# Optimization experiments

Measured on AMD Instinct MI355X. Metric: run time of the kernel, lower is better.

## Reference

```python
import jax, jax.numpy as jnp
import numpy as np

N_NODES = 100000
N_EDGES = 1600000
IN_C, HID_C, OUT_C = 128, 128, 64


def setup_inputs() -> dict:
    key = jax.random.key(0)
    ks = jax.random.split(key, 9)
    features = jax.random.normal(ks[0], (N_NODES, IN_C), dtype=jnp.float32)
    src = jax.random.randint(ks[1], (N_EDGES,), 0, N_NODES, dtype=jnp.int32)
    dst = jax.random.randint(ks[2], (N_EDGES,), 0, N_NODES, dtype=jnp.int32)
    def glorot(k, fan_in, fan_out):
        lim = float(np.sqrt(6.0 / (fan_in + fan_out)))
        return jax.random.uniform(k, (fan_in, fan_out), jnp.float32, -lim, lim)
    return {
        "features": features, "src": src, "dst": dst,
        "W1": glorot(ks[3], IN_C, HID_C), "b1": jnp.zeros((HID_C,), jnp.float32),
        "W2": glorot(ks[4], HID_C, HID_C), "b2": jnp.zeros((HID_C,), jnp.float32),
        "W3": glorot(ks[5], HID_C, OUT_C), "b3": jnp.zeros((OUT_C,), jnp.float32),
    }


def _graph_conv(x, src, dst, W, b, inv_sqrt_out, inv_sqrt_in):
    # DGL GraphConv, norm='both': h = D_in^{-1/2} A D_out^{-1/2} (x W) + b
    h = (x * inv_sqrt_out[:, None]) @ W            # [N, out]
    agg = jax.ops.segment_sum(h[src], dst, num_segments=N_NODES)
    return agg * inv_sqrt_in[:, None] + b


def reference(features, src, dst, W1, b1, W2, b2, W3, b3):
    ones = jnp.ones((N_EDGES,), jnp.float32)
    deg_out = jnp.clip(jax.ops.segment_sum(ones, src, num_segments=N_NODES), 1.0)
    deg_in = jnp.clip(jax.ops.segment_sum(ones, dst, num_segments=N_NODES), 1.0)
    iso, isi = deg_out ** -0.5, deg_in ** -0.5
    x = jax.nn.relu(_graph_conv(features, src, dst, W1, b1, iso, isi))
    x = jax.nn.relu(_graph_conv(x, src, dst, W2, b2, iso, isi))
    x = _graph_conv(x, src, dst, W3, b3, iso, isi)
    return jax.nn.log_softmax(x, axis=1)
```

## Files before the change

kernel.cpp:

```cpp
#include <hip/hip_runtime.h>
#include <hip/hip_bf16.h>

#define IN_C 128
#define HID_C 128
#define OUT_C 64

typedef unsigned short u16;
typedef unsigned int   u32;
typedef __attribute__((ext_vector_type(8))) short short8;
typedef __attribute__((ext_vector_type(4))) float f32x4;
typedef __attribute__((ext_vector_type(2))) float f32x2;

__device__ __forceinline__ u16 bf16_bits(float x) {
    __hip_bfloat16 h = __float2bfloat16(x);
    return *(u16*)&h;
}
__device__ __forceinline__ void split_hi_lo(float a, u16& hi, u16& lo) {
    __hip_bfloat16 h = __float2bfloat16(a);
    float hf = __bfloat162float(h);
    __hip_bfloat16 l = __float2bfloat16(a - hf);
    hi = *(u16*)&h; lo = *(u16*)&l;
}
__device__ __forceinline__ void pk_acc(f32x2& acc, u32 v) {
    f32x2 val;
    val.x = __uint_as_float(v << 16);
    val.y = __uint_as_float(v & 0xffff0000u);
    asm("v_pk_add_f32 %0, %0, %1" : "+v"(acc) : "v"(val));
}


__global__ __launch_bounds__(256)
void part_hist(const int* __restrict__ keys, int* __restrict__ bh,
               int E, int K, int NB) {
    const int b = blockIdx.x;
    extern __shared__ int lh[];
    for (int i = threadIdx.x; i < K; i += 256) lh[i] = 0;
    __syncthreads();
    const int lo = (int)((long long)E * b / NB);
    const int hi = (int)((long long)E * (b + 1) / NB);
    for (int i = lo + threadIdx.x; i < hi; i += 256)
        atomicAdd(&lh[keys[i] >> 8], 1);
    __syncthreads();
    for (int k = threadIdx.x; k < K; k += 256)
        bh[k * NB + b] = lh[k];
}

template <bool PACK>
__global__ __launch_bounds__(256)
void part_scatter(const int* __restrict__ keys, const int* __restrict__ other,
                  const int* __restrict__ ofs, u32* __restrict__ out,
                  int E, int K, int NB) {
    const int b = blockIdx.x;
    extern __shared__ int lcur[];
    for (int k = threadIdx.x; k < K; k += 256) lcur[k] = ofs[k * NB + b];
    __syncthreads();
    const int lo = (int)((long long)E * b / NB);
    const int hi = (int)((long long)E * (b + 1) / NB);
    for (int i = lo + threadIdx.x; i < hi; i += 256) {
        int key = keys[i];
        int p = atomicAdd(&lcur[key >> 8], 1);
        out[p] = PACK ? (((u32)other[i] << 8) | (u32)(key & 255)) : (u32)key;
    }
}

__global__ __launch_bounds__(256)
void bucket_count(const u32* __restrict__ pairs, const int* __restrict__ ofs,
                  int* __restrict__ cnt, int N, int NB, int K, int cap) {
    const int k = blockIdx.x;
    __shared__ int lc[256];
    lc[threadIdx.x] = 0;
    __syncthreads();
    const int s0 = ofs[k * NB];
    const int s1 = (k == K - 1) ? cap : ofs[(k + 1) * NB];
    for (int i = s0 + threadIdx.x; i < s1; i += 256)
        atomicAdd(&lc[pairs[i] & 255], 1);
    __syncthreads();
    const int node = k * 256 + threadIdx.x;
    if (node < N) cnt[node] = lc[threadIdx.x];
}

__global__ __launch_bounds__(256)
void bucket_fill(const u32* __restrict__ pairs, const int* __restrict__ ofs,
                 const int* __restrict__ row_start, int* __restrict__ csr,
                 int N, int NB, int K, int E) {
    const int k = blockIdx.x;
    __shared__ int lcur[256];
    const int node = k * 256 + threadIdx.x;
    lcur[threadIdx.x] = (node < N) ? row_start[node] : 0;
    __syncthreads();
    const int s0 = ofs[k * NB];
    const int s1 = (k == K - 1) ? E : ofs[(k + 1) * NB];
    for (int i = s0 + threadIdx.x; i < s1; i += 256) {
        u32 pr = pairs[i];
        int p = atomicAdd(&lcur[pr & 255], 1);
        csr[p] = (int)(pr >> 8);
    }
}


__global__ __launch_bounds__(256)
void scan_pass1(const int* __restrict__ in, int* __restrict__ blocksum, int M) {
    const int b = blockIdx.x, t = threadIdx.x;
    const int base = b * 1024 + t * 4;
    int s = 0;
#pragma unroll
    for (int j = 0; j < 4; ++j) {
        int idx = base + j;
        if (idx < M) s += in[idx];
    }
#pragma unroll
    for (int off = 32; off >= 1; off >>= 1) s += __shfl_xor(s, off);
    __shared__ int wsum[4];
    if ((t & 63) == 0) wsum[t >> 6] = s;
    __syncthreads();
    if (t == 0) blocksum[b] = wsum[0] + wsum[1] + wsum[2] + wsum[3];
}

__global__ __launch_bounds__(1024)
void scan_g2(int* __restrict__ a, int nb) {
    __shared__ int s[1024];
    const int t = threadIdx.x;
    int v = (t < nb) ? a[t] : 0;
    s[t] = v;
    __syncthreads();
    for (int off = 1; off < 1024; off <<= 1) {
        int x = (t >= off) ? s[t - off] : 0;
        __syncthreads();
        s[t] += x;
        __syncthreads();
    }
    if (t < nb) a[t] = s[t] - v;
}

__global__ __launch_bounds__(256)
void scan_g3(const int* __restrict__ in, const int* __restrict__ blockoff,
             int* __restrict__ out, int M) {
    __shared__ int ssum[256];
    const int b = blockIdx.x, t = threadIdx.x;
    const int base = b * 1024 + t * 4;
    int c[4];
#pragma unroll
    for (int j = 0; j < 4; ++j) {
        int idx = base + j;
        c[j] = (idx < M) ? in[idx] : 0;
    }
    const int tot = c[0] + c[1] + c[2] + c[3];
    ssum[t] = tot;
    __syncthreads();
    for (int off = 1; off < 256; off <<= 1) {
        int v = (t >= off) ? ssum[t - off] : 0;
        __syncthreads();
        ssum[t] += v;
        __syncthreads();
    }
    int run = blockoff[b] + ssum[t] - tot;
#pragma unroll
    for (int j = 0; j < 4; ++j) {
        int idx = base + j;
        if (idx < M) { out[idx] = run; run += c[j]; }
    }
}

__global__ __launch_bounds__(256)
void scan_pass3n(const int* __restrict__ cnt_in, const int* __restrict__ cnt_out,
                 const int* __restrict__ blockoff, int* __restrict__ row_start,
                 float* __restrict__ iso, float* __restrict__ isi, int N, int E) {
    __shared__ int ssum[256];
    const int b = blockIdx.x, t = threadIdx.x;
    const int base = b * 1024 + t * 4;
    int c[4];
#pragma unroll
    for (int j = 0; j < 4; ++j) {
        int idx = base + j;
        c[j] = (idx < N) ? cnt_in[idx] : 0;
    }
    const int tot = c[0] + c[1] + c[2] + c[3];
    ssum[t] = tot;
    __syncthreads();
    for (int off = 1; off < 256; off <<= 1) {
        int v = (t >= off) ? ssum[t - off] : 0;
        __syncthreads();
        ssum[t] += v;
        __syncthreads();
    }
    int run = blockoff[b] + ssum[t] - tot;
#pragma unroll
    for (int j = 0; j < 4; ++j) {
        int idx = base + j;
        if (idx < N) {
            row_start[idx] = run;
            run += c[j];
            int di = c[j] < 1 ? 1 : c[j];
            int co = cnt_out[idx];
            int dd = co < 1 ? 1 : co;
            isi[idx] = rsqrtf((float)di);
            iso[idx] = rsqrtf((float)dd);
        }
    }
    if (b == 0 && t == 0) row_start[N] = E;
}


__global__ __launch_bounds__(128)
void wt_prep_all(const float* __restrict__ W1, const float* __restrict__ W2,
                 const float* __restrict__ W3, u16* __restrict__ Wt1,
                 u16* __restrict__ Wt2, u16* __restrict__ Wt3) {
    const int b = blockIdx.x, k = threadIdx.x;
    if (b < 128)       Wt1[b * 128 + k] = bf16_bits(W1[k * 128 + b]);
    else if (b < 256)  { int c = b - 128; Wt2[c * 128 + k] = bf16_bits(W2[k * 128 + c]); }
    else               { int c = b - 256; Wt3[c * 128 + k] = bf16_bits(W3[k * 64 + c]); }
}

template <int C>
__device__ __forceinline__
void mfma_store(const u16* sAh, const u16* sAl, const u16* __restrict__ Wt,
                u16* __restrict__ H, int row0, int N, int t) {
    constexpr int NT = C / 16;
    const int wid = t >> 6, lane = t & 63;
    const int r0 = wid * 16;
    const int arow = r0 + (lane & 15);
    const int kb = (lane >> 4) * 8;

    f32x4 acc[NT];
#pragma unroll
    for (int i = 0; i < NT; ++i) acc[i] = (f32x4){0.f, 0.f, 0.f, 0.f};

    const u16* wbase = Wt + (size_t)(lane & 15) * 128 + kb;

#pragma unroll
    for (int kk = 0; kk < 4; ++kk) {
        short8 ah = *(const short8*)(&sAh[arow * 136 + kk * 32 + kb]);
        short8 al = *(const short8*)(&sAl[arow * 136 + kk * 32 + kb]);
#pragma unroll
        for (int ct = 0; ct < NT; ++ct) {
            short8 bf = *(const short8*)(wbase + ct * 16 * 128 + kk * 32);
            acc[ct] = __builtin_amdgcn_mfma_f32_16x16x32_bf16(ah, bf, acc[ct], 0, 0, 0);
            acc[ct] = __builtin_amdgcn_mfma_f32_16x16x32_bf16(al, bf, acc[ct], 0, 0, 0);
        }
    }

    const int rbase = row0 + r0 + (lane >> 4) * 4;
#pragma unroll
    for (int ct = 0; ct < NT; ++ct) {
        int gcol = ct * 16 + (lane & 15);
#pragma unroll
        for (int r = 0; r < 4; ++r) {
            int grow = rbase + r;
            if (grow < N) H[(size_t)grow * C + gcol] = bf16_bits(acc[ct][r]);
        }
    }
}


__global__ __launch_bounds__(256)
void gemm1_fused(const float* __restrict__ X, const float* __restrict__ iso,
                 const u16* __restrict__ Wt, u16* __restrict__ H, int N) {
    __shared__ u16 sAh[64 * 136];
    __shared__ u16 sAl[64 * 136];
    const int t = threadIdx.x;
    const int row0 = blockIdx.x * 64;

    for (int i = t; i < 2048; i += 256) {
        int r = i >> 5, kv = (i & 31) << 2;
        int gr = row0 + r;
        if (gr >= N) gr = N - 1;
        float s = iso[gr];
        float4 x = *(const float4*)(X + (size_t)gr * 128 + kv);
        u16 h0, l0, h1, l1, h2, l2, h3, l3;
        split_hi_lo(x.x * s, h0, l0);
        split_hi_lo(x.y * s, h1, l1);
        split_hi_lo(x.z * s, h2, l2);
        split_hi_lo(x.w * s, h3, l3);
        uint2 hp = make_uint2((u32)h0 | ((u32)h1 << 16), (u32)h2 | ((u32)h3 << 16));
        uint2 lp = make_uint2((u32)l0 | ((u32)l1 << 16), (u32)l2 | ((u32)l3 << 16));
        *(uint2*)(&sAh[r * 136 + kv]) = hp;
        *(uint2*)(&sAl[r * 136 + kv]) = lp;
    }
    __syncthreads();
    mfma_store<128>(sAh, sAl, Wt, H, row0, N, t);
}


template <int C>
__global__ __launch_bounds__(256)
void gemm_mfma(const u16* __restrict__ Ah, const u16* __restrict__ Al,
               const u16* __restrict__ Wt, u16* __restrict__ H, int N) {
    __shared__ u16 sAh[64 * 136];
    __shared__ u16 sAl[64 * 136];
    const int t = threadIdx.x;
    const int row0 = blockIdx.x * 64;

    for (int c = t; c < 1024; c += 256) {
        int r = c >> 4, kc = c & 15;
        int gr = row0 + r;
        if (gr >= N) gr = N - 1;
        *(uint4*)(&sAh[r * 136 + kc * 8]) = *(const uint4*)(Ah + (size_t)gr * 128 + kc * 8);
        *(uint4*)(&sAl[r * 136 + kc * 8]) = *(const uint4*)(Al + (size_t)gr * 128 + kc * 8);
    }
    __syncthreads();
    mfma_store<C>(sAh, sAl, Wt, H, row0, N, t);
}


__device__ __forceinline__
f32x2 gather128(const u16* __restrict__ Hin, const int* __restrict__ csr_src,
                int rs, int re, int lane) {
    f32x2 acc; acc.x = 0.f; acc.y = 0.f;
    int e = rs;
    while (e < re) {
        int nloc = re - e;
        if (nloc > 64) nloc = 64;
        int idx = (lane < nloc) ? csr_src[e + lane] : 0;
        int j = 0;
        for (; j + 16 <= nloc; j += 16) {
            u32 v[16];
#pragma unroll
            for (int q = 0; q < 16; ++q) {
                int s = __builtin_amdgcn_readlane(idx, j + q);
                v[q] = *(const u32*)(Hin + (size_t)s * 128 + lane * 2);
            }
#pragma unroll
            for (int q = 0; q < 16; ++q) pk_acc(acc, v[q]);
        }
        for (; j + 4 <= nloc; j += 4) {
            u32 v[4];
#pragma unroll
            for (int q = 0; q < 4; ++q) {
                int s = __builtin_amdgcn_readlane(idx, j + q);
                v[q] = *(const u32*)(Hin + (size_t)s * 128 + lane * 2);
            }
#pragma unroll
            for (int q = 0; q < 4; ++q) pk_acc(acc, v[q]);
        }
        for (; j < nloc; ++j) {
            int s = __builtin_amdgcn_readlane(idx, j);
            pk_acc(acc, *(const u32*)(Hin + (size_t)s * 128 + lane * 2));
        }
        e += nloc;
    }
    return acc;
}


__global__ __launch_bounds__(256)
void agg_relu(const u16* __restrict__ H, const int* __restrict__ row_start,
              const int* __restrict__ csr_src, const float* __restrict__ isi,
              const float* __restrict__ iso, const float* __restrict__ bias,
              u16* __restrict__ Ah, u16* __restrict__ Al, int N) {
    const int wid  = (int)((blockIdx.x * (size_t)blockDim.x + threadIdx.x) >> 6);
    const int lane = threadIdx.x & 63;
    if (wid >= N) return;
    const int rs = row_start[wid];
    const int re = row_start[wid + 1];

    f32x2 acc = gather128(H, csr_src, rs, re, lane);

    float2 b = *(const float2*)(bias + lane * 2);
    const float sc = isi[wid], so = iso[wid];
    float o0 = fmaxf(acc.x * sc + b.x, 0.f) * so;
    float o1 = fmaxf(acc.y * sc + b.y, 0.f) * so;
    u16 h0, l0, h1, l1;
    split_hi_lo(o0, h0, l0);
    split_hi_lo(o1, h1, l1);
    ((u32*)Ah)[(size_t)wid * 64 + lane] = (u32)h0 | ((u32)h1 << 16);
    ((u32*)Al)[(size_t)wid * 64 + lane] = (u32)l0 | ((u32)l1 << 16);
}


__global__ __launch_bounds__(256)
void agg_final(const u16* __restrict__ H, const int* __restrict__ row_start,
               const int* __restrict__ csr_src, const float* __restrict__ isi,
               const float* __restrict__ bias, float* __restrict__ Out, int N) {
    const int wid  = (int)((blockIdx.x * (size_t)blockDim.x + threadIdx.x) >> 6);
    const int lane = threadIdx.x & 63;
    if (wid >= N) return;
    const int rs = row_start[wid];
    const int re = row_start[wid + 1];
    const float sc = isi[wid];

    float a = 0.f;
    int e = rs;
    while (e < re) {
        int nloc = re - e;
        if (nloc > 64) nloc = 64;
        int idx = (lane < nloc) ? csr_src[e + lane] : 0;
        int j = 0;
        for (; j + 8 <= nloc; j += 8) {
            u32 v[8];
#pragma unroll
            for (int q = 0; q < 8; ++q) {
                int s = __builtin_amdgcn_readlane(idx, j + q);
                v[q] = H[(size_t)s * 64 + lane];
            }
#pragma unroll
            for (int q = 0; q < 8; ++q) a += __uint_as_float(v[q] << 16);
        }
        for (; j + 4 <= nloc; j += 4) {
            u32 v[4];
#pragma unroll
            for (int q = 0; q < 4; ++q) {
                int s = __builtin_amdgcn_readlane(idx, j + q);
                v[q] = H[(size_t)s * 64 + lane];
            }
#pragma unroll
            for (int q = 0; q < 4; ++q) a += __uint_as_float(v[q] << 16);
        }
        for (; j < nloc; ++j) {
            int s = __builtin_amdgcn_readlane(idx, j);
            a += __uint_as_float((u32)H[(size_t)s * 64 + lane] << 16);
        }
        e += nloc;
    }
    float v = a * sc + bias[lane];
    float m = v;
#pragma unroll
    for (int off = 32; off >= 1; off >>= 1) m = fmaxf(m, __shfl_xor(m, off));
    float ex = expf(v - m);
    float ss = ex;
#pragma unroll
    for (int off = 32; off >= 1; off >>= 1) ss += __shfl_xor(ss, off);
    v = (v - m) - logf(ss);
    Out[(size_t)wid * 64 + lane] = v;
}


extern "C" void kernel_launch(void* const* d_in, const int* in_sizes, int n_in,
                              void* d_out, int out_size, void* d_ws, size_t ws_size,
                              hipStream_t stream) {
    const float* features = (const float*)d_in[0];
    const int*   src      = (const int*)d_in[1];
    const int*   dst      = (const int*)d_in[2];
    const float* W1       = (const float*)d_in[3];
    const float* b1       = (const float*)d_in[4];
    const float* W2       = (const float*)d_in[5];
    const float* b2       = (const float*)d_in[6];
    const float* W3       = (const float*)d_in[7];
    const float* b3       = (const float*)d_in[8];
    float*       out      = (float*)d_out;

    const int N  = in_sizes[0] / IN_C;
    const int E  = in_sizes[1];
    const int K  = (N + 255) >> 8;
    const int NB = 256;
    const int M  = 2 * K * NB;
    const int nbe = (M + 1023) / 1024;
    const int nb  = (N + 1023) / 1024;

    char* ws = (char*)d_ws;
    const size_t SLOT = 400128;
    int*   cnt_out   = (int*)(ws + 0 * SLOT);
    int*   cnt_in    = (int*)(ws + 1 * SLOT);
    int*   row_start = (int*)(ws + 2 * SLOT);
    float* iso       = (float*)(ws + 3 * SLOT);
    float* isi       = (float*)(ws + 4 * SLOT);
    int*   blocksum  = (int*)(ws + 5 * SLOT);
    int*   eblocksum = blocksum + 2048;
    int*   csr       = (int*)(ws + 6 * SLOT);
    char*  p         = ws + 6 * SLOT + 6400000;
    int*   BH        = (int*)p;
    int*   OFS       = (int*)(p + 1000000);
    u32*   pairs     = (u32*)(p + 2000000);
    u16*   Hb        = (u16*)(p + 14800000);
    u16*   Ah        = (u16*)(p + 40400000);
    u16*   Al        = (u16*)(p + 66000000);
    u16*   Wt1       = (u16*)(p + 91600000);
    u16*   Wt2       = Wt1 + 128 * 128;
    u16*   Wt3       = Wt2 + 128 * 128;

    const size_t ldsK = (size_t)K * sizeof(int);

    part_hist<<<NB, 256, ldsK, stream>>>(dst, BH,           E, K, NB);
    part_hist<<<NB, 256, ldsK, stream>>>(src, BH + K * NB,  E, K, NB);
    scan_pass1<<<nbe, 256, 0, stream>>>(BH, eblocksum, M);
    scan_g2<<<1, 1024, 0, stream>>>(eblocksum, nbe);
    scan_g3<<<nbe, 256, 0, stream>>>(BH, eblocksum, OFS, M);
    part_scatter<true ><<<NB, 256, ldsK, stream>>>(dst, src, OFS,          pairs, E, K, NB);
    part_scatter<false><<<NB, 256, ldsK, stream>>>(src, src, OFS + K * NB, pairs, E, K, NB);
    bucket_count<<<K, 256, 0, stream>>>(pairs, OFS,          cnt_in,  N, NB, K, E);
    bucket_count<<<K, 256, 0, stream>>>(pairs, OFS + K * NB, cnt_out, N, NB, K, 2 * E);
    scan_pass1<<<nb, 256, 0, stream>>>(cnt_in, blocksum, N);
    scan_g2<<<1, 1024, 0, stream>>>(blocksum, nb);
    scan_pass3n<<<nb, 256, 0, stream>>>(cnt_in, cnt_out, blocksum, row_start, iso, isi, N, E);
    bucket_fill<<<K, 256, 0, stream>>>(pairs, OFS, row_start, csr, N, NB, K, E);

    wt_prep_all<<<320, 128, 0, stream>>>(W1, W2, W3, Wt1, Wt2, Wt3);

    const int gblocks = (N + 63) / 64;
    const int ablocks = (int)(((size_t)N * 64 + 255) / 256);

    gemm1_fused<<<gblocks, 256, 0, stream>>>(features, iso, Wt1, Hb, N);
    agg_relu<<<ablocks, 256, 0, stream>>>(Hb, row_start, csr, isi, iso, b1, Ah, Al, N);
    gemm_mfma<128><<<gblocks, 256, 0, stream>>>(Ah, Al, Wt2, Hb, N);
    agg_relu<<<ablocks, 256, 0, stream>>>(Hb, row_start, csr, isi, iso, b2, Ah, Al, N);
    gemm_mfma<64><<<gblocks, 256, 0, stream>>>(Ah, Al, Wt3, Hb, N);
    agg_final<<<ablocks, 256, 0, stream>>>(Hb, row_start, csr, isi, b3, out, N);
}
```

Baseline: 373.0 us.

## Merge src/dst partition kernels and reuse bucket offsets for row starts

Fuses the src and dst histogram, scatter and bucket-count kernels into single launches that process both key arrays per pass. The separate scan of in-degree counts is dropped: row starts are taken from the bucket offsets already computed (OFS at bucket b*4), so two scan launches disappear. The change also adds nontemporal loads and stores on streaming data and unrolls the final aggregation gather to 16. Together these cut launch count and redundant passes over the edge arrays, at the cost of more LDS per block in the fused partition kernels.

Measured after the change: 378.2 us. Within noise of the previous version (+1.4%).

```diff
diff --git a/kernel.cpp b/kernel.cpp
--- a/kernel.cpp
+++ b/kernel.cpp
@@ -30,43 +30,57 @@
 
 
 __global__ __launch_bounds__(256)
-void part_hist(const int* __restrict__ keys, int* __restrict__ bh,
-               int E, int K, int NB) {
+void part_hist2(const int* __restrict__ src, const int* __restrict__ dst,
+                int* __restrict__ bh, int E, int K, int NB) {
     const int b = blockIdx.x;
     extern __shared__ int lh[];
-    for (int i = threadIdx.x; i < K; i += 256) lh[i] = 0;
-    __syncthreads();
-    const int lo = (int)((long long)E * b / NB);
-    const int hi = (int)((long long)E * (b + 1) / NB);
-    for (int i = lo + threadIdx.x; i < hi; i += 256)
-        atomicAdd(&lh[keys[i] >> 8], 1);
-    __syncthreads();
-    for (int k = threadIdx.x; k < K; k += 256)
-        bh[k * NB + b] = lh[k];
-}
-
-template <bool PACK>
-__global__ __launch_bounds__(256)
-void part_scatter(const int* __restrict__ keys, const int* __restrict__ other,
-                  const int* __restrict__ ofs, u32* __restrict__ out,
-                  int E, int K, int NB) {
-    const int b = blockIdx.x;
-    extern __shared__ int lcur[];
-    for (int k = threadIdx.x; k < K; k += 256) lcur[k] = ofs[k * NB + b];
+    for (int i = threadIdx.x; i < 2 * K; i += 256) lh[i] = 0;
     __syncthreads();
     const int lo = (int)((long long)E * b / NB);
     const int hi = (int)((long long)E * (b + 1) / NB);
     for (int i = lo + threadIdx.x; i < hi; i += 256) {
-        int key = keys[i];
-        int p = atomicAdd(&lcur[key >> 8], 1);
-        out[p] = PACK ? (((u32)other[i] << 8) | (u32)(key & 255)) : (u32)key;
-    }
-}
-
-__global__ __launch_bounds__(256)
-void bucket_count(const u32* __restrict__ pairs, const int* __restrict__ ofs,
-                  int* __restrict__ cnt, int N, int NB, int K, int cap) {
-    const int k = blockIdx.x;
+        int d = __builtin_nontemporal_load(&dst[i]);
+        int s = __builtin_nontemporal_load(&src[i]);
+        atomicAdd(&lh[d >> 8], 1);
+        atomicAdd(&lh[K + (s >> 8)], 1);
+    }
+    __syncthreads();
+    for (int k = threadIdx.x; k < K; k += 256) {
+        bh[k * NB + b]            = lh[k];
+        bh[(K + k) * NB + b]      = lh[K + k];
+    }
+}
+
+__global__ __launch_bounds__(256)
+void part_scatter2(const int* __restrict__ src, const int* __restrict__ dst,
+                   const int* __restrict__ ofs, u32* __restrict__ pairs,
+                   int E, int K, int NB) {
+    const int b = blockIdx.x;
+    extern __shared__ int lcur[];
+    for (int k = threadIdx.x; k < 2 * K; k += 256) lcur[k] = ofs[k * NB + b];
+    __syncthreads();
+    const int lo = (int)((long long)E * b / NB);
+    const int hi = (int)((long long)E * (b + 1) / NB);
+    for (int i = lo + threadIdx.x; i < hi; i += 256) {
+        int d = __builtin_nontemporal_load(&dst[i]);
+        int s = __builtin_nontemporal_load(&src[i]);
+        int p1 = atomicAdd(&lcur[d >> 8], 1);
+        pairs[p1] = ((u32)s << 8) | (u32)(d & 255);
+        int p2 = atomicAdd(&lcur[K + (s >> 8)], 1);
+        pairs[p2] = (u32)s;
+    }
+}
+
+__global__ __launch_bounds__(256)
+void bucket_count2(const u32* __restrict__ pairs, const int* __restrict__ OFS,
+                   int* __restrict__ cnt_in, int* __restrict__ cnt_out,
+                   int N, int NB, int K, int E) {
+    const int kk = blockIdx.x;
+    const bool is_src = kk >= K;
+    const int k = is_src ? kk - K : kk;
+    const int* ofs = OFS + (is_src ? K * NB : 0);
+    int* cnt = is_src ? cnt_out : cnt_in;
+    const int cap = is_src ? 2 * E : E;
     __shared__ int lc[256];
     lc[threadIdx.x] = 0;
     __syncthreads();
@@ -163,8 +177,9 @@
 
 __global__ __launch_bounds__(256)
 void scan_pass3n(const int* __restrict__ cnt_in, const int* __restrict__ cnt_out,
-                 const int* __restrict__ blockoff, int* __restrict__ row_start,
-                 float* __restrict__ iso, float* __restrict__ isi, int N, int E) {
+                 const int* __restrict__ OFS, int* __restrict__ row_start,
+                 float* __restrict__ iso, float* __restrict__ isi,
+                 int N, int E, int NB) {
     __shared__ int ssum[256];
     const int b = blockIdx.x, t = threadIdx.x;
     const int base = b * 1024 + t * 4;
@@ -183,7 +198,7 @@
         ssum[t] += v;
         __syncthreads();
     }
-    int run = blockoff[b] + ssum[t] - tot;
+    int run = OFS[(b << 2) * NB] + ssum[t] - tot;
 #pragma unroll
     for (int j = 0; j < 4; ++j) {
         int idx = base + j;
@@ -310,7 +325,7 @@
     while (e < re) {
         int nloc = re - e;
         if (nloc > 64) nloc = 64;
-        int idx = (lane < nloc) ? csr_src[e + lane] : 0;
+        int idx = (lane < nloc) ? __builtin_nontemporal_load(&csr_src[e + lane]) : 0;
         int j = 0;
         for (; j + 16 <= nloc; j += 16) {
             u32 v[16];
@@ -383,17 +398,17 @@
     while (e < re) {
         int nloc = re - e;
         if (nloc > 64) nloc = 64;
-        int idx = (lane < nloc) ? csr_src[e + lane] : 0;
+        int idx = (lane < nloc) ? __builtin_nontemporal_load(&csr_src[e + lane]) : 0;
         int j = 0;
-        for (; j + 8 <= nloc; j += 8) {
-            u32 v[8];
-#pragma unroll
-            for (int q = 0; q < 8; ++q) {
+        for (; j + 16 <= nloc; j += 16) {
+            u32 v[16];
+#pragma unroll
+            for (int q = 0; q < 16; ++q) {
                 int s = __builtin_amdgcn_readlane(idx, j + q);
                 v[q] = H[(size_t)s * 64 + lane];
             }
 #pragma unroll
-            for (int q = 0; q < 8; ++q) a += __uint_as_float(v[q] << 16);
+            for (int q = 0; q < 16; ++q) a += __uint_as_float(v[q] << 16);
         }
         for (; j + 4 <= nloc; j += 4) {
             u32 v[4];
@@ -420,7 +435,7 @@
 #pragma unroll
     for (int off = 32; off >= 1; off >>= 1) ss += __shfl_xor(ss, off);
     v = (v - m) - logf(ss);
-    Out[(size_t)wid * 64 + lane] = v;
+    __builtin_nontemporal_store(v, &Out[(size_t)wid * 64 + lane]);
 }
 
 
@@ -453,8 +468,7 @@
     int*   row_start = (int*)(ws + 2 * SLOT);
     float* iso       = (float*)(ws + 3 * SLOT);
     float* isi       = (float*)(ws + 4 * SLOT);
-    int*   blocksum  = (int*)(ws + 5 * SLOT);
-    int*   eblocksum = blocksum + 2048;
+    int*   eblocksum = (int*)(ws + 5 * SLOT);
     int*   csr       = (int*)(ws + 6 * SLOT);
     char*  p         = ws + 6 * SLOT + 6400000;
     int*   BH        = (int*)p;
@@ -467,20 +481,15 @@
     u16*   Wt2       = Wt1 + 128 * 128;
     u16*   Wt3       = Wt2 + 128 * 128;
 
-    const size_t ldsK = (size_t)K * sizeof(int);
-
-    part_hist<<<NB, 256, ldsK, stream>>>(dst, BH,           E, K, NB);
-    part_hist<<<NB, 256, ldsK, stream>>>(src, BH + K * NB,  E, K, NB);
+    const size_t ldsK2 = (size_t)(2 * K) * sizeof(int);
+
+    part_hist2<<<NB, 256, ldsK2, stream>>>(src, dst, BH, E, K, NB);
     scan_pass1<<<nbe, 256, 0, stream>>>(BH, eblocksum, M);
     scan_g2<<<1, 1024, 0, stream>>>(eblocksum, nbe);
     scan_g3<<<nbe, 256, 0, stream>>>(BH, eblocksum, OFS, M);
-    part_scatter<true ><<<NB, 256, ldsK, stream>>>(dst, src, OFS,          pairs, E, K, NB);
-    part_scatter<false><<<NB, 256, ldsK, stream>>>(src, src, OFS + K * NB, pairs, E, K, NB);
-    bucket_count<<<K, 256, 0, stream>>>(pairs, OFS,          cnt_in,  N, NB, K, E);
-    bucket_count<<<K, 256, 0, stream>>>(pairs, OFS + K * NB, cnt_out, N, NB, K, 2 * E);
-    scan_pass1<<<nb, 256, 0, stream>>>(cnt_in, blocksum, N);
-    scan_g2<<<1, 1024, 0, stream>>>(blocksum, nb);
-    scan_pass3n<<<nb, 256, 0, stream>>>(cnt_in, cnt_out, blocksum, row_start, iso, isi, N, E);
+    part_scatter2<<<NB, 256, ldsK2, stream>>>(src, dst, OFS, pairs, E, K, NB);
+    bucket_count2<<<2 * K, 256, 0, stream>>>(pairs, OFS, cnt_in, cnt_out, N, NB, K, E);
+    scan_pass3n<<<nb, 256, 0, stream>>>(cnt_in, cnt_out, OFS, row_start, iso, isi, N, E, NB);
     bucket_fill<<<K, 256, 0, stream>>>(pairs, OFS, row_start, csr, N, NB, K, E);
 
     wt_prep_all<<<320, 128, 0, stream>>>(W1, W2, W3, Wt1, Wt2, Wt3);
```
